# Kernel optimization log

Hardware: AMD Instinct MI355X
Metric: run time of the kernel (lower is better)

## Reference

```python
import jax, jax.numpy as jnp
import numpy as np

N = 100000   # nodes
F = 128      # feature dim (== numEdges ctor arg)
H = 64       # hidden_dim
E = 1600000  # edges (avg degree 16)


def setup_inputs() -> dict:
    key = jax.random.key(0)
    ks = jax.random.split(key, 8)
    x = jax.random.normal(ks[0], (N, F), dtype=jnp.float32)
    edge_index = jax.random.randint(ks[1], (2, E), 0, N)
    sF = 1.0 / np.sqrt(F)
    sH = 1.0 / np.sqrt(H)
    conv_W = jax.random.normal(ks[2], (F, F), dtype=jnp.float32) * sF  # GCNConv linear weight
    conv_b = jnp.zeros((F,), dtype=jnp.float32)
    w1 = jax.random.normal(ks[3], (H, F), dtype=jnp.float32) * sF
    b1 = jnp.zeros((H,), dtype=jnp.float32)
    w2 = jax.random.normal(ks[4], (H, H), dtype=jnp.float32) * sH
    b2 = jnp.zeros((H,), dtype=jnp.float32)
    w3 = jax.random.normal(ks[5], (1, H), dtype=jnp.float32) * sH
    b3 = jnp.zeros((1,), dtype=jnp.float32)
    return dict(x=x, edge_index=edge_index, conv_W=conv_W, conv_b=conv_b,
                w1=w1, b1=b1, w2=w2, b2=b2, w3=w3, b3=b3)


def reference(x, edge_index, conv_W, conv_b, w1, b1, w2, b2, w3, b3):
    n = x.shape[0]
    # --- GCNConv: D^{-1/2}(A+I)D^{-1/2} X W + b ---
    xw = x @ conv_W.T                                   # [N, F]
    loops = jnp.arange(n)
    src = jnp.concatenate([edge_index[0], loops])       # add self-loops
    dst = jnp.concatenate([edge_index[1], loops])
    deg = jax.ops.segment_sum(jnp.ones(src.shape[0], xw.dtype), dst, num_segments=n)
    dinv = jnp.where(deg > 0, jax.lax.rsqrt(deg), 0.0)
    norm = dinv[src] * dinv[dst]                        # [E+N]
    h = jax.ops.segment_sum(xw[src] * norm[:, None], dst, num_segments=n) + conv_b  # [N, F]
    # --- MedianAggregation (index=None -> single segment, 'lower' interpolation) ---
    med = jnp.sort(h, axis=0)[(n - 1) // 2][None, :]    # [1, F]
    # --- tanh MLP ---
    a = jnp.tanh(med @ w1.T + b1)
    a = jnp.tanh(a @ w2.T + b2)
    return a @ w3.T + b3                                # [1, 1]
```

## Files before the change

### kernel.cpp

```cpp
#include <hip/hip_runtime.h>
#include <math.h>


#define CAP    24576
#define CCAP   96
#define DSTR   32
#define OVCAP  4096
#define BCAP   4608
#define NBKMAX 400
#define CH     4096

typedef __attribute__((ext_vector_type(8))) short short8;
typedef __attribute__((ext_vector_type(4))) float f32x4;
typedef __attribute__((ext_vector_type(8))) _Float16 half8;
typedef __attribute__((ext_vector_type(2))) _Float16 half2v;

__device__ __forceinline__ unsigned ordKey(float x) {
    unsigned u = __float_as_uint(x);
    return (u & 0x80000000u) ? ~u : (u | 0x80000000u);
}
__device__ __forceinline__ float keyToFloat(unsigned k) {
    unsigned bits = (k & 0x80000000u) ? (k & 0x7FFFFFFFu) : ~k;
    return __uint_as_float(bits);
}
__device__ __forceinline__ unsigned short f2bf(float f) {
    unsigned u = __float_as_uint(f);
    return (unsigned short)((u + 0x7FFFu + ((u >> 16) & 1u)) >> 16);
}

__global__ void k_init(int* __restrict__ cursor, int* __restrict__ below,
                       int* __restrict__ candCnt, int* __restrict__ ovCnt,
                       const float* __restrict__ W, short* __restrict__ Whi,
                       short* __restrict__ Wlo, int nbk) {
    if (blockIdx.x == 1) {
        for (int idx = threadIdx.x; idx < 16384; idx += 256) {
            int j = idx & 7, lane = (idx >> 3) & 63;
            int t = (idx >> 9) & 7, s = idx >> 12;
            int row = t * 16 + (lane & 15);
            int k = s * 32 + (lane >> 4) * 8 + j;
            float w = W[row * 128 + k];
            unsigned short hb = f2bf(w);
            float hf = __uint_as_float((unsigned)hb << 16);
            Whi[idx] = (short)hb;
            Wlo[idx] = (short)f2bf(w - hf);
        }
        return;
    }
    int t = threadIdx.x;
    for (int i = t; i < nbk; i += 256) cursor[i] = 0;
    if (t < 128) { below[t] = 0; candCnt[t] = 0; }
    if (t == 0) ovCnt[0] = 0;
}

__global__ __launch_bounds__(256) void k_binGemm(
        const float* __restrict__ x, const short* __restrict__ Whi,
        const short* __restrict__ Wlo, _Float16* __restrict__ xw, int n, int GB,
        const int* __restrict__ src, const int* __restrict__ dst, int E,
        int* __restrict__ cursor, int2* __restrict__ binned,
        int* __restrict__ ovCnt, int2* __restrict__ ovBuf, int nbk) {
    __shared__ char smem[39168];
    const int t = threadIdx.x;
    if ((int)blockIdx.x < GB) {
        float* trn = (float*)smem;
        const int lane = t & 63, wv = t >> 6;
        const int quad = lane >> 4, m = lane & 15;
        const int rowBase = blockIdx.x * 64 + wv * 16;
        const int r = rowBase + m;
        const int rl = r < n ? r : (n - 1);
        f32x4 acc[8];
        #pragma unroll
        for (int q = 0; q < 8; q++) acc[q] = (f32x4){0.f, 0.f, 0.f, 0.f};
        #pragma unroll
        for (int s = 0; s < 4; s++) {
            const float* xp = x + (size_t)rl * 128 + s * 32 + quad * 8;
            float4 p0 = *(const float4*)xp;
            float4 p1 = *(const float4*)(xp + 4);
            float f[8] = {p0.x, p0.y, p0.z, p0.w, p1.x, p1.y, p1.z, p1.w};
            short8 ah, al;
            #pragma unroll
            for (int j = 0; j < 8; j++) {
                unsigned short hb = f2bf(f[j]);
                float hf = __uint_as_float((unsigned)hb << 16);
                ah[j] = (short)hb;
                al[j] = (short)f2bf(f[j] - hf);
            }
            #pragma unroll
            for (int q = 0; q < 8; q++) {
                short8 bh = *(const short8*)(Whi + (((s * 8 + q) * 64 + lane) << 3));
                short8 bl = *(const short8*)(Wlo + (((s * 8 + q) * 64 + lane) << 3));
                acc[q] = __builtin_amdgcn_mfma_f32_16x16x32_bf16(ah, bh, acc[q], 0, 0, 0);
                acc[q] = __builtin_amdgcn_mfma_f32_16x16x32_bf16(al, bh, acc[q], 0, 0, 0);
                acc[q] = __builtin_amdgcn_mfma_f32_16x16x32_bf16(ah, bl, acc[q], 0, 0, 0);
            }
        }
        float* tw = trn + wv * (16 * 132);
        #pragma unroll
        for (int q = 0; q < 8; q++)
            #pragma unroll
            for (int e = 0; e < 4; e++)
                tw[(quad * 4 + e) * 132 + q * 16 + m] = acc[q][e];
        #pragma unroll
        for (int i = 0; i < 4; i++) {
            int row = i * 4 + (lane >> 4);
            int c8 = lane & 15;
            const float* tp = tw + row * 132 + c8 * 8;
            float4 p0 = *(const float4*)tp;
            float4 p1 = *(const float4*)(tp + 4);
            half8 o;
            o[0] = (_Float16)p0.x; o[1] = (_Float16)p0.y;
            o[2] = (_Float16)p0.z; o[3] = (_Float16)p0.w;
            o[4] = (_Float16)p1.x; o[5] = (_Float16)p1.y;
            o[6] = (_Float16)p1.z; o[7] = (_Float16)p1.w;
            int grow = rowBase + row;
            if (grow < n) *(half8*)(xw + (size_t)grow * 128 + c8 * 8) = o;
        }
    } else {
        int2* stage = (int2*)smem;
        int* hist  = (int*)(smem + 32768);
        int* gbase = hist + NBKMAX;
        int* hist2 = gbase + NBKMAX;
        int* sbase = hist2 + NBKMAX;
        const int e0 = ((int)blockIdx.x - GB) * CH;
        const int len = min(CH, E - e0);
        for (int i = t; i < nbk; i += 256) { hist[i] = 0; hist2[i] = 0; }
        __syncthreads();
        for (int k = t; k < len; k += 256) {
            int s = src[e0 + k], d = dst[e0 + k];
            stage[k] = make_int2(s, d);
            atomicAdd(&hist[d >> 8], 1);
        }
        __syncthreads();
        for (int i = t; i < nbk; i += 256) {
            int c = hist[i];
            if (c) {
                int g = atomicAdd(&cursor[i], c);
                if (g + c <= BCAP) gbase[i] = g;
                else {
                    gbase[i] = -1;
                    sbase[i] = atomicAdd(ovCnt, c);
                }
            }
        }
        __syncthreads();
        for (int k = t; k < len; k += 256) {
            int2 e = stage[k];
            int b = e.y >> 8;
            int p = atomicAdd(&hist2[b], 1);
            int g = gbase[b];
            if (g >= 0) binned[(size_t)b * BCAP + g + p] = e;
            else {
                int o = sbase[b] + p;
                if (o < OVCAP) ovBuf[o] = make_int2(e.y, e.x);
            }
        }
    }
}

__global__ __launch_bounds__(256) void k_build(int2* __restrict__ binned,
                                               const int* __restrict__ cursor,
                                               float* __restrict__ dinv,
                                               unsigned char* __restrict__ deg8,
                                               int* __restrict__ ovCnt,
                                               int2* __restrict__ ovBuf, int n) {
    __shared__ int ladj[256 * DSTR];
    __shared__ int lcnt[256];
    const int b = blockIdx.x, t = threadIdx.x;
    const int cnt = min(cursor[b], BCAP);
    const size_t e0 = (size_t)b * BCAP;
    lcnt[t] = 0;
    __syncthreads();
    for (int k = t; k < cnt; k += 256) {
        int2 e = binned[e0 + k];
        int li = e.y & 255;
        int pos = atomicAdd(&lcnt[li], 1);
        if (pos < DSTR) ladj[li * DSTR + pos] = e.x;
        else {
            int o = atomicAdd(ovCnt, 1);
            if (o < OVCAP) ovBuf[o] = make_int2(e.y, e.x);
        }
    }
    __syncthreads();
    int4* adjOut = (int4*)((int*)binned + e0 * 2);
    const int4* lsrc4 = (const int4*)ladj;
    for (int i = t; i < 2048; i += 256) adjOut[i] = lsrc4[i];
    int node = b * 256 + t;
    if (node < n) {
        int deg = lcnt[t];
        dinv[node] = (float)(1.0 / sqrt((double)(deg + 1)));
        deg8[node] = (unsigned char)(deg < DSTR ? deg : DSTR);
    }
}

__global__ __launch_bounds__(256) void k_agg(const _Float16* __restrict__ xw,
                                             const unsigned char* __restrict__ deg8,
                                             const int* __restrict__ adjAll,
                                             const float* __restrict__ dinv,
                                             const float* __restrict__ conv_b,
                                             float* __restrict__ h, int n) {
    const int d = blockIdx.x * 4 + (threadIdx.x >> 6);
    if (d >= n) return;
    const int lane = threadIdx.x & 63;
    const int l32 = lane & 31;
    const int degB = deg8[d];
    const float dd = dinv[d];
    const int* adjRow = adjAll + (size_t)(d >> 8) * (BCAP * 2) + (d & 255) * DSTR;
    int aj = adjRow[l32];
    bool ev = (lane < 32) && (l32 < degB);
    int ajs = ev ? aj : 0;
    float dv = ev ? dinv[ajs] : 0.f;
    const half2v* xwv = (const half2v*)xw;
    half2v a = xwv[(size_t)d * 64 + lane];
    float ax = dd * dd * (float)a.x, ay = dd * dd * (float)a.y;
    int j = 0;
    for (; j + 8 <= degB; j += 8) {
        int s[8];
        float w[8];
        #pragma unroll
        for (int q = 0; q < 8; q++) {
            s[q] = __shfl(ajs, j + q, 64);
            w[q] = dd * __shfl(dv, j + q, 64);
        }
        #pragma unroll
        for (int q = 0; q < 8; q++) {
            half2v v = xwv[(size_t)s[q] * 64 + lane];
            ax += w[q] * (float)v.x;
            ay += w[q] * (float)v.y;
        }
    }
    if (j < degB) {
        int s[8];
        float w[8];
        #pragma unroll
        for (int q = 0; q < 8; q++) {
            int idx = j + q;
            bool ok = idx < degB;
            int lsrc = ok ? idx : 0;
            int sv = __shfl(ajs, lsrc, 64);
            float wv = dd * __shfl(dv, lsrc, 64);
            s[q] = ok ? sv : 0;
            w[q] = ok ? wv : 0.f;
        }
        #pragma unroll
        for (int q = 0; q < 8; q++) {
            half2v v = xwv[(size_t)s[q] * 64 + lane];
            ax += w[q] * (float)v.x;
            ay += w[q] * (float)v.y;
        }
    }
    float2 cb = ((const float2*)conv_b)[lane];
    float2 o;
    o.x = ax + cb.x;
    o.y = ay + cb.y;
    ((float2*)h)[(size_t)d * 64 + lane] = o;
}

__global__ void k_spill(const int2* __restrict__ ovBuf, const int* __restrict__ ovCnt,
                        const _Float16* __restrict__ xw, const float* __restrict__ dinv,
                        float* __restrict__ h) {
    int m = ovCnt[0];
    if (m > OVCAP) m = OVCAP;
    int t = threadIdx.x;
    for (int i = blockIdx.x; i < m; i += gridDim.x) {
        int2 e = ovBuf[i];
        float w = dinv[e.x] * dinv[e.y];
        if (t < 128)
            atomicAdd(&h[(size_t)e.x * 128 + t],
                      w * (float)xw[(size_t)e.y * 128 + t]);
    }
}

__global__ __launch_bounds__(256) void k_sample(const float* __restrict__ h, int n,
                                                unsigned* __restrict__ Lkey,
                                                unsigned* __restrict__ Ukey) {
    __shared__ int hist[2048];
    __shared__ int wsum[4];
    const int c = blockIdx.x, t = threadIdx.x;
    for (int i = t; i < 2048; i += 256) hist[i] = 0;
    __syncthreads();
    const int ns = (n + 31) >> 5;
    for (int i = t; i < ns; i += 256) {
        float v = h[(size_t)(i << 5) * 128 + c];
        atomicAdd(&hist[ordKey(v) >> 21], 1);
    }
    __syncthreads();
    int ps = 0;
    #pragma unroll
    for (int b = 0; b < 8; b++) ps += hist[t * 8 + b];
    const int lane = t & 63, wv = t >> 6;
    int sc = ps;
    #pragma unroll
    for (int off = 1; off < 64; off <<= 1) {
        int y = __shfl_up(sc, off, 64);
        if (lane >= off) sc += y;
    }
    if (lane == 63) wsum[wv] = sc;
    __syncthreads();
    int wbase = 0;
    for (int ww = 0; ww < wv; ww++) wbase += wsum[ww];
    const int excl = wbase + sc - ps;
    const int sMid = (ns - 1) >> 1;
    const int delta = (int)(4.0f * sqrtf((float)ns)) + 1;
    int sLo = sMid - delta; if (sLo < 0) sLo = 0;
    int sHi = sMid + delta; if (sHi > ns - 1) sHi = ns - 1;
    if (sLo >= excl && sLo < excl + ps) {
        int rem = sLo - excl, b = t * 8;
        for (;; b++) { int cc = hist[b]; if (rem < cc) break; rem -= cc; }
        Lkey[c] = (unsigned)b << 21;
    }
    if (sHi >= excl && sHi < excl + ps) {
        int rem = sHi - excl, b = t * 8;
        for (;; b++) { int cc = hist[b]; if (rem < cc) break; rem -= cc; }
        Ukey[c] = (((unsigned)(b + 1)) << 21) - 1u;
    }
}

__global__ __launch_bounds__(256) void k_collect(const float* __restrict__ h, int total4,
                                                 const unsigned* __restrict__ Lkey,
                                                 const unsigned* __restrict__ Ukey,
                                                 int* __restrict__ below,
                                                 int* __restrict__ candCnt,
                                                 float* __restrict__ cand) {
    __shared__ float buf[128 * CCAP];
    __shared__ int cN[128], cB[128];
    const int t = threadIdx.x;
    for (int i = t; i < 128; i += 256) { cN[i] = 0; cB[i] = 0; }
    __syncthreads();
    const int stride = gridDim.x * blockDim.x;
    const int i0 = blockIdx.x * blockDim.x + t;
    const int jb = (i0 << 2) & 127;
    const unsigned L0 = Lkey[jb],     U0 = Ukey[jb];
    const unsigned L1 = Lkey[jb + 1], U1 = Ukey[jb + 1];
    const unsigned L2 = Lkey[jb + 2], U2 = Ukey[jb + 2];
    const unsigned L3 = Lkey[jb + 3], U3 = Ukey[jb + 3];
    int b0 = 0, b1 = 0, b2 = 0, b3 = 0;
    const float4* hv = (const float4*)h;
    for (int i = i0; i < total4; i += stride) {
        float4 v = hv[i];
        unsigned u;
        u = ordKey(v.x);
        if (u < L0) b0++;
        else if (u <= U0) { int p = atomicAdd(&cN[jb], 1); if (p < CCAP) buf[jb * CCAP + p] = v.x; }
        u = ordKey(v.y);
        if (u < L1) b1++;
        else if (u <= U1) { int p = atomicAdd(&cN[jb + 1], 1); if (p < CCAP) buf[(jb + 1) * CCAP + p] = v.y; }
        u = ordKey(v.z);
        if (u < L2) b2++;
        else if (u <= U2) { int p = atomicAdd(&cN[jb + 2], 1); if (p < CCAP) buf[(jb + 2) * CCAP + p] = v.z; }
        u = ordKey(v.w);
        if (u < L3) b3++;
        else if (u <= U3) { int p = atomicAdd(&cN[jb + 3], 1); if (p < CCAP) buf[(jb + 3) * CCAP + p] = v.w; }
    }
    if (b0) atomicAdd(&cB[jb], b0);
    if (b1) atomicAdd(&cB[jb + 1], b1);
    if (b2) atomicAdd(&cB[jb + 2], b2);
    if (b3) atomicAdd(&cB[jb + 3], b3);
    __syncthreads();
    if (t < 128) {
        if (cB[t]) atomicAdd(&below[t], cB[t]);
        int nn = cN[t] < CCAP ? cN[t] : CCAP;
        if (nn) {
            int base = atomicAdd(&candCnt[t], nn);
            for (int k = 0; k < nn && base + k < CAP; k++)
                cand[(size_t)t * CAP + base + k] = buf[t * CCAP + k];
        }
    }
}

__global__ __launch_bounds__(256) void k_final(const float* __restrict__ cand,
                                               const int* __restrict__ candCnt,
                                               const int* __restrict__ below, int n,
                                               float* __restrict__ med) {
    __shared__ int hist[2048];
    __shared__ unsigned sPre;
    __shared__ int sRank;
    const int c = blockIdx.x, t = threadIdx.x;
    int cnt = candCnt[c]; if (cnt > CAP) cnt = CAP;
    const float* cp = cand + (size_t)c * CAP;
    if (t == 0) {
        int r = (n - 1) / 2 - below[c];
        if (r < 0) r = 0;
        if (r >= cnt) r = cnt - 1;
        sRank = r;
        sPre = 0u;
    }
    __syncthreads();
    #pragma unroll
    for (int round = 0; round < 3; round++) {
        const int nb = (round == 2) ? 1024 : 2048;
        for (int i = t; i < nb; i += 256) hist[i] = 0;
        __syncthreads();
        for (int i = t; i < cnt; i += 256) {
            unsigned u = ordKey(cp[i]);
            bool ok;
            int bin;
            if (round == 0)      { ok = true;                      bin = u >> 21; }
            else if (round == 1) { ok = (u >> 21) == (sPre >> 21); bin = (u >> 10) & 2047; }
            else                 { ok = (u >> 10) == (sPre >> 10); bin = u & 1023; }
            if (ok) atomicAdd(&hist[bin], 1);
        }
        __syncthreads();
        if (t < 64) {
            const int per = nb >> 6;
            int ps = 0;
            for (int b = t * per; b < t * per + per; b++) ps += hist[b];
            int sc = ps;
            #pragma unroll
            for (int off = 1; off < 64; off <<= 1) {
                int y = __shfl_up(sc, off, 64);
                if (t >= off) sc += y;
            }
            int excl = sc - ps;
            int r = sRank;
            if (excl <= r && r < sc) {
                int b = t * per, rem = r - excl;
                for (;; b++) {
                    int cc = hist[b];
                    if (rem < cc) break;
                    rem -= cc;
                }
                if (round == 0)      sPre = (unsigned)b << 21;
                else if (round == 1) sPre |= (unsigned)b << 10;
                else                 sPre |= (unsigned)b;
                sRank = rem;
            }
        }
        __syncthreads();
    }
    if (t == 0) med[c] = keyToFloat(sPre);
}

__global__ void k_mlp(const float* __restrict__ med,
                      const float* __restrict__ w1, const float* __restrict__ b1,
                      const float* __restrict__ w2, const float* __restrict__ b2,
                      const float* __restrict__ w3, const float* __restrict__ b3,
                      float* __restrict__ out) {
    __shared__ float m[128], a1[64], a2[64];
    int t = threadIdx.x;
    if (t < 128) m[t] = med[t];
    __syncthreads();
    if (t < 64) {
        float acc = b1[t];
        for (int f = 0; f < 128; f++) acc += m[f] * w1[t * 128 + f];
        a1[t] = tanhf(acc);
    }
    __syncthreads();
    if (t < 64) {
        float acc = b2[t];
        for (int f = 0; f < 64; f++) acc += a1[f] * w2[t * 64 + f];
        a2[t] = tanhf(acc);
    }
    __syncthreads();
    if (t == 0) {
        float acc = b3[0];
        for (int f = 0; f < 64; f++) acc += a2[f] * w3[f];
        out[0] = acc;
    }
}

extern "C" void kernel_launch(void* const* d_in, const int* in_sizes, int n_in,
                              void* d_out, int out_size, void* d_ws, size_t ws_size,
                              hipStream_t stream) {
    const float* x      = (const float*)d_in[0];
    const int*   ei     = (const int*)d_in[1];
    const float* conv_W = (const float*)d_in[2];
    const float* conv_b = (const float*)d_in[3];
    const float* w1 = (const float*)d_in[4];
    const float* b1 = (const float*)d_in[5];
    const float* w2 = (const float*)d_in[6];
    const float* b2 = (const float*)d_in[7];
    const float* w3 = (const float*)d_in[8];
    const float* b3 = (const float*)d_in[9];

    const int N = in_sizes[0] / 128;
    const int E = in_sizes[1] / 2;
    const int* src = ei;
    const int* dst = ei + E;
    const int NBK = (N + 255) / 256;

    char* p = (char*)d_ws;
    auto alloc = [&](size_t bytes) -> char* {
        char* q = p;
        p += (bytes + 255) & ~(size_t)255;
        return q;
    };
    _Float16* xw  = (_Float16*)alloc((size_t)N * 128 * 2);
    float* h      = (float*)alloc((size_t)N * 128 * 4);
    int2*  binned = (int2*)alloc((size_t)NBK * BCAP * 8);
    float* cand   = (float*)binned;
    float* dinv   = (float*)alloc((size_t)N * 4);
    unsigned char* deg8 = (unsigned char*)alloc((size_t)N);
    int*   cursor = (int*)alloc((size_t)NBK * 4);
    short* Whi    = (short*)alloc(16384 * 2);
    short* Wlo    = (short*)alloc(16384 * 2);
    int2*  ovBuf  = (int2*)alloc((size_t)OVCAP * 8);
    int*   ovCnt  = (int*)alloc(256);
    unsigned* Lkey = (unsigned*)alloc(128 * 4);
    unsigned* Ukey = (unsigned*)alloc(128 * 4);
    int*   below   = (int*)alloc(128 * 4);
    int*   candCnt = (int*)alloc(128 * 4);
    float* med     = (float*)alloc(128 * 4);

    const int GB   = (N + 63) / 64;
    const int BINB = (E + CH - 1) / CH;

    k_init<<<2, 256, 0, stream>>>(cursor, below, candCnt, ovCnt, conv_W, Whi, Wlo, NBK);
    k_binGemm<<<GB + BINB, 256, 0, stream>>>(x, Whi, Wlo, xw, N, GB,
                                             src, dst, E, cursor, binned,
                                             ovCnt, ovBuf, NBK);
    k_build<<<NBK, 256, 0, stream>>>(binned, cursor, dinv, deg8, ovCnt, ovBuf, N);
    k_agg<<<(N + 3) / 4, 256, 0, stream>>>(xw, deg8, (const int*)binned, dinv,
                                           conv_b, h, N);
    k_spill<<<16, 128, 0, stream>>>(ovBuf, ovCnt, xw, dinv, h);
    k_sample<<<128, 256, 0, stream>>>(h, N, Lkey, Ukey);
    k_collect<<<1024, 256, 0, stream>>>(h, N * 32, Lkey, Ukey, below, candCnt, cand);
    k_final<<<128, 256, 0, stream>>>(cand, candCnt, below, N, med);
    k_mlp<<<1, 128, 0, stream>>>(med, w1, b1, w2, b2, w3, b3, (float*)d_out);
}
```

Measured before the change: 326.3 us.

## Fuse aggregation with median candidate selection, avoiding full h materialization

Instead of writing the full N×128 fp32 aggregated feature matrix and rereading it for sampling and candidate collection, the change aggregates only every 32nd node for the histogram sample. It then recomputes aggregation for all nodes inside a fused kernel that directly classifies each value against the sample bounds. Nodes with degree above the adjacency stride are deferred to a spill kernel that finishes their sums, including overflow edges, before classifying them. This removes a large write and two reads of h, in exchange for an extra gather pass over sampled nodes and a linear scan of the overflow buffer per spilled node.

New measurement: 318.6 us. 2.4% less time.

```diff
diff --git a/kernel.cpp b/kernel.cpp
--- a/kernel.cpp
+++ b/kernel.cpp
@@ -3,12 +3,14 @@
 
 
 #define CAP    24576
-#define CCAP   96
+#define CCF    32
 #define DSTR   32
 #define OVCAP  4096
+#define SPCAP  2048
 #define BCAP   4608
 #define NBKMAX 400
 #define CH     4096
+#define NPB    64
 
 typedef __attribute__((ext_vector_type(8))) short short8;
 typedef __attribute__((ext_vector_type(4))) float f32x4;
@@ -49,7 +51,7 @@
     int t = threadIdx.x;
     for (int i = t; i < nbk; i += 256) cursor[i] = 0;
     if (t < 128) { below[t] = 0; candCnt[t] = 0; }
-    if (t == 0) ovCnt[0] = 0;
+    if (t == 0) { ovCnt[0] = 0; ovCnt[1] = 0; }
 }
 
 __global__ __launch_bounds__(256) void k_binGemm(
@@ -161,7 +163,8 @@
                                                float* __restrict__ dinv,
                                                unsigned char* __restrict__ deg8,
                                                int* __restrict__ ovCnt,
-                                               int2* __restrict__ ovBuf, int n) {
+                                               int2* __restrict__ ovBuf,
+                                               int* __restrict__ spillNodes, int n) {
     __shared__ int ladj[256 * DSTR];
     __shared__ int lcnt[256];
     const int b = blockIdx.x, t = threadIdx.x;
@@ -187,21 +190,27 @@
     if (node < n) {
         int deg = lcnt[t];
         dinv[node] = (float)(1.0 / sqrt((double)(deg + 1)));
-        deg8[node] = (unsigned char)(deg < DSTR ? deg : DSTR);
-    }
-}
-
-__global__ __launch_bounds__(256) void k_agg(const _Float16* __restrict__ xw,
-                                             const unsigned char* __restrict__ deg8,
-                                             const int* __restrict__ adjAll,
-                                             const float* __restrict__ dinv,
-                                             const float* __restrict__ conv_b,
-                                             float* __restrict__ h, int n) {
-    const int d = blockIdx.x * 4 + (threadIdx.x >> 6);
-    if (d >= n) return;
+        deg8[node] = (unsigned char)(deg < 255 ? deg : 255);
+        if (deg > DSTR) {
+            int p = atomicAdd(ovCnt + 1, 1);
+            if (p < SPCAP) spillNodes[p] = node;
+        }
+    }
+}
+
+__global__ __launch_bounds__(256) void k_aggS(const _Float16* __restrict__ xw,
+                                              const unsigned char* __restrict__ deg8,
+                                              const int* __restrict__ adjAll,
+                                              const float* __restrict__ dinv,
+                                              const float* __restrict__ conv_b,
+                                              float* __restrict__ hS, int n, int ns) {
+    const int si = blockIdx.x * 4 + (threadIdx.x >> 6);
+    if (si >= ns) return;
+    const int d = si << 5;
     const int lane = threadIdx.x & 63;
     const int l32 = lane & 31;
-    const int degB = deg8[d];
+    int degT = deg8[d];
+    const int degB = degT < DSTR ? degT : DSTR;
     const float dd = dinv[d];
     const int* adjRow = adjAll + (size_t)(d >> 8) * (BCAP * 2) + (d & 255) * DSTR;
     int aj = adjRow[l32];
@@ -251,25 +260,10 @@
     float2 o;
     o.x = ax + cb.x;
     o.y = ay + cb.y;
-    ((float2*)h)[(size_t)d * 64 + lane] = o;
-}
-
-__global__ void k_spill(const int2* __restrict__ ovBuf, const int* __restrict__ ovCnt,
-                        const _Float16* __restrict__ xw, const float* __restrict__ dinv,
-                        float* __restrict__ h) {
-    int m = ovCnt[0];
-    if (m > OVCAP) m = OVCAP;
-    int t = threadIdx.x;
-    for (int i = blockIdx.x; i < m; i += gridDim.x) {
-        int2 e = ovBuf[i];
-        float w = dinv[e.x] * dinv[e.y];
-        if (t < 128)
-            atomicAdd(&h[(size_t)e.x * 128 + t],
-                      w * (float)xw[(size_t)e.y * 128 + t]);
-    }
-}
-
-__global__ __launch_bounds__(256) void k_sample(const float* __restrict__ h, int n,
+    ((float2*)hS)[(size_t)si * 64 + lane] = o;
+}
+
+__global__ __launch_bounds__(256) void k_sample(const float* __restrict__ hS, int n,
                                                 unsigned* __restrict__ Lkey,
                                                 unsigned* __restrict__ Ukey) {
     __shared__ int hist[2048];
@@ -279,7 +273,7 @@
     __syncthreads();
     const int ns = (n + 31) >> 5;
     for (int i = t; i < ns; i += 256) {
-        float v = h[(size_t)(i << 5) * 128 + c];
+        float v = hS[(size_t)i * 128 + c];
         atomicAdd(&hist[ordKey(v) >> 21], 1);
     }
     __syncthreads();
@@ -314,54 +308,140 @@
     }
 }
 
-__global__ __launch_bounds__(256) void k_collect(const float* __restrict__ h, int total4,
-                                                 const unsigned* __restrict__ Lkey,
-                                                 const unsigned* __restrict__ Ukey,
-                                                 int* __restrict__ below,
-                                                 int* __restrict__ candCnt,
-                                                 float* __restrict__ cand) {
-    __shared__ float buf[128 * CCAP];
-    __shared__ int cN[128], cB[128];
+__global__ __launch_bounds__(256) void k_aggSel(
+        const _Float16* __restrict__ xw, const unsigned char* __restrict__ deg8,
+        const int* __restrict__ adjAll, const float* __restrict__ dinv,
+        const float* __restrict__ conv_b, const unsigned* __restrict__ Lkey,
+        const unsigned* __restrict__ Ukey, int* __restrict__ below,
+        int* __restrict__ candCnt, float* __restrict__ cand, int n) {
+    __shared__ float buf[128 * CCF];
+    __shared__ int cN[128];
+    __shared__ int bl[128];
     const int t = threadIdx.x;
-    for (int i = t; i < 128; i += 256) { cN[i] = 0; cB[i] = 0; }
-    __syncthreads();
-    const int stride = gridDim.x * blockDim.x;
-    const int i0 = blockIdx.x * blockDim.x + t;
-    const int jb = (i0 << 2) & 127;
-    const unsigned L0 = Lkey[jb],     U0 = Ukey[jb];
-    const unsigned L1 = Lkey[jb + 1], U1 = Ukey[jb + 1];
-    const unsigned L2 = Lkey[jb + 2], U2 = Ukey[jb + 2];
-    const unsigned L3 = Lkey[jb + 3], U3 = Ukey[jb + 3];
-    int b0 = 0, b1 = 0, b2 = 0, b3 = 0;
-    const float4* hv = (const float4*)h;
-    for (int i = i0; i < total4; i += stride) {
-        float4 v = hv[i];
-        unsigned u;
-        u = ordKey(v.x);
-        if (u < L0) b0++;
-        else if (u <= U0) { int p = atomicAdd(&cN[jb], 1); if (p < CCAP) buf[jb * CCAP + p] = v.x; }
-        u = ordKey(v.y);
-        if (u < L1) b1++;
-        else if (u <= U1) { int p = atomicAdd(&cN[jb + 1], 1); if (p < CCAP) buf[(jb + 1) * CCAP + p] = v.y; }
-        u = ordKey(v.z);
-        if (u < L2) b2++;
-        else if (u <= U2) { int p = atomicAdd(&cN[jb + 2], 1); if (p < CCAP) buf[(jb + 2) * CCAP + p] = v.z; }
-        u = ordKey(v.w);
-        if (u < L3) b3++;
-        else if (u <= U3) { int p = atomicAdd(&cN[jb + 3], 1); if (p < CCAP) buf[(jb + 3) * CCAP + p] = v.w; }
-    }
-    if (b0) atomicAdd(&cB[jb], b0);
-    if (b1) atomicAdd(&cB[jb + 1], b1);
-    if (b2) atomicAdd(&cB[jb + 2], b2);
-    if (b3) atomicAdd(&cB[jb + 3], b3);
+    const int lane = t & 63, wv = t >> 6;
+    const int l32 = lane & 31;
+    if (t < 128) { cN[t] = 0; bl[t] = 0; }
+    __syncthreads();
+    const int c0 = lane * 2, c1 = c0 + 1;
+    const unsigned L0 = Lkey[c0], U0 = Ukey[c0];
+    const unsigned L1 = Lkey[c1], U1 = Ukey[c1];
+    const float2 cb = ((const float2*)conv_b)[lane];
+    const half2v* xwv = (const half2v*)xw;
+    int cnt0 = 0, cnt1 = 0;
+    const int dBase = blockIdx.x * NPB + wv * 16;
+    for (int k = 0; k < 16; k++) {
+        const int d = dBase + k;
+        if (d >= n) break;
+        const int degB = deg8[d];
+        if (degB > DSTR) continue;
+        const float dd = dinv[d];
+        const int* adjRow = adjAll + (size_t)(d >> 8) * (BCAP * 2) + (d & 255) * DSTR;
+        int aj = adjRow[l32];
+        bool ev = (lane < 32) && (l32 < degB);
+        int ajs = ev ? aj : 0;
+        float dv = ev ? dinv[ajs] : 0.f;
+        half2v a = xwv[(size_t)d * 64 + lane];
+        float ax = dd * dd * (float)a.x, ay = dd * dd * (float)a.y;
+        int j = 0;
+        for (; j + 8 <= degB; j += 8) {
+            int s[8];
+            float w[8];
+            #pragma unroll
+            for (int q = 0; q < 8; q++) {
+                s[q] = __shfl(ajs, j + q, 64);
+                w[q] = dd * __shfl(dv, j + q, 64);
+            }
+            #pragma unroll
+            for (int q = 0; q < 8; q++) {
+                half2v v = xwv[(size_t)s[q] * 64 + lane];
+                ax += w[q] * (float)v.x;
+                ay += w[q] * (float)v.y;
+            }
+        }
+        if (j < degB) {
+            int s[8];
+            float w[8];
+            #pragma unroll
+            for (int q = 0; q < 8; q++) {
+                int idx = j + q;
+                bool ok = idx < degB;
+                int lsrc = ok ? idx : 0;
+                int sv = __shfl(ajs, lsrc, 64);
+                float wv = dd * __shfl(dv, lsrc, 64);
+                s[q] = ok ? sv : 0;
+                w[q] = ok ? wv : 0.f;
+            }
+            #pragma unroll
+            for (int q = 0; q < 8; q++) {
+                half2v v = xwv[(size_t)s[q] * 64 + lane];
+                ax += w[q] * (float)v.x;
+                ay += w[q] * (float)v.y;
+            }
+        }
+        const float vx = ax + cb.x, vy = ay + cb.y;
+        const unsigned u0 = ordKey(vx), u1 = ordKey(vy);
+        if (u0 < L0) cnt0++;
+        else if (u0 <= U0) {
+            int p = atomicAdd(&cN[c0], 1);
+            if (p < CCF) buf[c0 * CCF + p] = vx;
+            else { int g = atomicAdd(&candCnt[c0], 1); if (g < CAP) cand[(size_t)c0 * CAP + g] = vx; }
+        }
+        if (u1 < L1) cnt1++;
+        else if (u1 <= U1) {
+            int p = atomicAdd(&cN[c1], 1);
+            if (p < CCF) buf[c1 * CCF + p] = vy;
+            else { int g = atomicAdd(&candCnt[c1], 1); if (g < CAP) cand[(size_t)c1 * CAP + g] = vy; }
+        }
+    }
+    if (cnt0) atomicAdd(&bl[c0], cnt0);
+    if (cnt1) atomicAdd(&bl[c1], cnt1);
     __syncthreads();
     if (t < 128) {
-        if (cB[t]) atomicAdd(&below[t], cB[t]);
-        int nn = cN[t] < CCAP ? cN[t] : CCAP;
+        if (bl[t]) atomicAdd(&below[t], bl[t]);
+        int nn = cN[t] < CCF ? cN[t] : CCF;
         if (nn) {
             int base = atomicAdd(&candCnt[t], nn);
-            for (int k = 0; k < nn && base + k < CAP; k++)
-                cand[(size_t)t * CAP + base + k] = buf[t * CCAP + k];
+            for (int k2 = 0; k2 < nn && base + k2 < CAP; k2++)
+                cand[(size_t)t * CAP + base + k2] = buf[t * CCF + k2];
+        }
+    }
+}
+
+__global__ void k_spillAgg(const _Float16* __restrict__ xw,
+                           const int* __restrict__ spillNodes,
+                           const unsigned char* __restrict__ deg8,
+                           const int* __restrict__ adjAll,
+                           const float* __restrict__ dinv,
+                           const float* __restrict__ conv_b,
+                           const int2* __restrict__ ovBuf,
+                           const int* __restrict__ ovCnt,
+                           const unsigned* __restrict__ Lkey,
+                           const unsigned* __restrict__ Ukey,
+                           int* __restrict__ below, int* __restrict__ candCnt,
+                           float* __restrict__ cand) {
+    int m = ovCnt[0];  if (m > OVCAP) m = OVCAP;
+    int sp = ovCnt[1]; if (sp > SPCAP) sp = SPCAP;
+    const int t = threadIdx.x;
+    for (int i = blockIdx.x; i < sp; i += gridDim.x) {
+        const int d = spillNodes[i];
+        const float dd = dinv[d];
+        float acc = dd * dd * (float)xw[(size_t)d * 128 + t];
+        const int* adjRow = adjAll + (size_t)(d >> 8) * (BCAP * 2) + (d & 255) * DSTR;
+        for (int j = 0; j < DSTR; j++) {
+            int a = adjRow[j];
+            acc += dd * dinv[a] * (float)xw[(size_t)a * 128 + t];
+        }
+        for (int k = 0; k < m; k++) {
+            int2 e = ovBuf[k];
+            if (e.x == d)
+                acc += dd * dinv[e.y] * (float)xw[(size_t)e.y * 128 + t];
+        }
+        const float v = acc + conv_b[t];
+        const unsigned u = ordKey(v);
+        if (u < Lkey[t]) atomicAdd(&below[t], 1);
+        else if (u <= Ukey[t]) {
+            int g = atomicAdd(&candCnt[t], 1);
+            if (g < CAP) cand[(size_t)t * CAP + g] = v;
         }
     }
 }
@@ -476,6 +556,7 @@
     const int* src = ei;
     const int* dst = ei + E;
     const int NBK = (N + 255) / 256;
+    const int NS  = (N + 31) >> 5;
 
     char* p = (char*)d_ws;
     auto alloc = [&](size_t bytes) -> char* {
@@ -484,9 +565,9 @@
         return q;
     };
     _Float16* xw  = (_Float16*)alloc((size_t)N * 128 * 2);
-    float* h      = (float*)alloc((size_t)N * 128 * 4);
     int2*  binned = (int2*)alloc((size_t)NBK * BCAP * 8);
-    float* cand   = (float*)binned;
+    float* cand   = (float*)alloc((size_t)128 * CAP * 4);
+    float* hS     = (float*)alloc((size_t)NS * 128 * 4);
     float* dinv   = (float*)alloc((size_t)N * 4);
     unsigned char* deg8 = (unsigned char*)alloc((size_t)N);
     int*   cursor = (int*)alloc((size_t)NBK * 4);
@@ -494,6 +575,7 @@
     short* Wlo    = (short*)alloc(16384 * 2);
     int2*  ovBuf  = (int2*)alloc((size_t)OVCAP * 8);
     int*   ovCnt  = (int*)alloc(256);
+    int*   spillNodes = (int*)alloc((size_t)SPCAP * 4);
     unsigned* Lkey = (unsigned*)alloc(128 * 4);
     unsigned* Ukey = (unsigned*)alloc(128 * 4);
     int*   below   = (int*)alloc(128 * 4);
@@ -507,12 +589,17 @@
     k_binGemm<<<GB + BINB, 256, 0, stream>>>(x, Whi, Wlo, xw, N, GB,
                                              src, dst, E, cursor, binned,
                                              ovCnt, ovBuf, NBK);
-    k_build<<<NBK, 256, 0, stream>>>(binned, cursor, dinv, deg8, ovCnt, ovBuf, N);
-    k_agg<<<(N + 3) / 4, 256, 0, stream>>>(xw, deg8, (const int*)binned, dinv,
-                                           conv_b, h, N);
-    k_spill<<<16, 128, 0, stream>>>(ovBuf, ovCnt, xw, dinv, h);
-    k_sample<<<128, 256, 0, stream>>>(h, N, Lkey, Ukey);
-    k_collect<<<1024, 256, 0, stream>>>(h, N * 32, Lkey, Ukey, below, candCnt, cand);
+    k_build<<<NBK, 256, 0, stream>>>(binned, cursor, dinv, deg8, ovCnt, ovBuf,
+                                     spillNodes, N);
+    k_aggS<<<(NS + 3) / 4, 256, 0, stream>>>(xw, deg8, (const int*)binned, dinv,
+                                             conv_b, hS, N, NS);
+    k_sample<<<128, 256, 0, stream>>>(hS, N, Lkey, Ukey);
+    k_aggSel<<<(N + NPB - 1) / NPB, 256, 0, stream>>>(xw, deg8, (const int*)binned,
+                                                      dinv, conv_b, Lkey, Ukey,
+                                                      below, candCnt, cand, N);
+    k_spillAgg<<<16, 128, 0, stream>>>(xw, spillNodes, deg8, (const int*)binned,
+                                       dinv, conv_b, ovBuf, ovCnt, Lkey, Ukey,
+                                       below, candCnt, cand);
     k_final<<<128, 256, 0, stream>>>(cand, candCnt, below, N, med);
     k_mlp<<<1, 128, 0, stream>>>(med, w1, b1, w2, b2, w3, b3, (float*)d_out);
 }
```
